# Performance work log

Hardware: AMD Instinct MI355X
Metric: run time of the kernel (lower is better)

The kernel has to match this reference:

```python
import jax, jax.numpy as jnp
import numpy as np

CH = 512
GROUPS = 32
EPS = 1e-5
B, H, W = 4, 64, 64


def setup_inputs() -> dict:
    key = jax.random.key(0)
    ks = jax.random.split(key, 6)
    s = 1.0 / np.sqrt(CH)  # conv2d default init scale (approx, uniform fan-in)
    return {
        "x": jax.random.normal(ks[0], (B, CH, H, W), dtype=jnp.float32),
        "norm_w": jnp.ones((CH,), jnp.float32),
        "norm_b": jnp.zeros((CH,), jnp.float32),
        "q_w": jax.random.normal(ks[1], (CH, CH), jnp.float32) * s,
        "q_b": jnp.zeros((CH,), jnp.float32),
        "k_w": jax.random.normal(ks[2], (CH, CH), jnp.float32) * s,
        "k_b": jnp.zeros((CH,), jnp.float32),
        "v_w": jax.random.normal(ks[3], (CH, CH), jnp.float32) * s,
        "v_b": jnp.zeros((CH,), jnp.float32),
        "proj_w": jax.random.normal(ks[4], (CH, CH), jnp.float32) * s,
        "proj_b": jnp.zeros((CH,), jnp.float32),
    }


def _group_norm(x, w, b):
    # x: [B, C, H, W]; 32 groups over channel dim
    bsz, c, h, wd = x.shape
    xg = x.reshape(bsz, GROUPS, c // GROUPS, h, wd)
    mean = xg.mean(axis=(2, 3, 4), keepdims=True)
    var = xg.var(axis=(2, 3, 4), keepdims=True)
    xg = (xg - mean) * jax.lax.rsqrt(var + EPS)
    x = xg.reshape(bsz, c, h, wd)
    return x * w[None, :, None, None] + b[None, :, None, None]


def _conv1x1(x, w, b):
    # x: [B, C, H, W], w: [O, C] -> [B, O, H, W]
    return jnp.einsum('bchw,oc->bohw', x, w) + b[None, :, None, None]


def reference(x, norm_w, norm_b, q_w, q_b, k_w, k_b, v_w, v_b, proj_w, proj_b):
    h = _group_norm(x, norm_w, norm_b)
    b, c, hh, ww = h.shape
    n = hh * ww
    q = _conv1x1(h, q_w, q_b).reshape(b, c, n).transpose(0, 2, 1)  # [b, n, c]
    k = _conv1x1(h, k_w, k_b).reshape(b, c, n)                     # [b, c, n]
    v = _conv1x1(h, v_w, v_b).reshape(b, c, n).transpose(0, 2, 1)  # [b, n, c]
    attn = jnp.einsum('bnc,bcm->bnm', q, k) * (c ** -0.5)          # [b, n, n]
    attn = jax.nn.softmax(attn, axis=-1)
    out = jnp.einsum('bnm,bmc->bnc', attn, v)                      # [b, n, c]
    out = out.transpose(0, 2, 1).reshape(b, c, hh, ww)
    return x + _conv1x1(out, proj_w, proj_b)
```

## Files before the change

### kernel.cpp

```cpp
#include <hip/hip_runtime.h>

#define NB 4
#define CH 512
#define NPIX 4096
#define GSZ 16
#define KVB 32
#define NT (NPIX / KVB)
#define DYN_LDS 136192
#define GEMM_LDS 65536

typedef __attribute__((ext_vector_type(8))) short bf16x8;
typedef __attribute__((ext_vector_type(4))) short bf16x4;
typedef __attribute__((ext_vector_type(4))) float f32x4;

#define MFMA __builtin_amdgcn_mfma_f32_16x16x32_bf16

static __device__ __forceinline__ short f2bf(float f) {
  unsigned u = __builtin_bit_cast(unsigned, f);
  u += 0x7fffu + ((u >> 16) & 1u);
  return (short)(u >> 16);
}

static __device__ __forceinline__ float bperm_f(int srclane, float v) {
  int r = __builtin_amdgcn_ds_bpermute(srclane << 2, __builtin_bit_cast(int, v));
  return __builtin_bit_cast(float, r);
}

typedef __attribute__((address_space(1))) unsigned glob_u32;
typedef __attribute__((address_space(3))) unsigned lds_u32;
static __device__ __forceinline__ void gl_lds16(const void* g, void* l) {
  __builtin_amdgcn_global_load_lds((const glob_u32*)g, (lds_u32*)l, 16, 0, 0);
}

__global__ __launch_bounds__(256) void wconv_kernel(
    const float* __restrict__ qw, const float* __restrict__ kw,
    const float* __restrict__ vw, const float* __restrict__ pw,
    short* __restrict__ wstack, short* __restrict__ wp) {
  int idx = (blockIdx.x * 256 + threadIdx.x) * 4;
  int mat = idx >> 18;
  int off = idx & 262143;
  const float* src = (mat == 0) ? qw : (mat == 1) ? kw : (mat == 2) ? vw : pw;
  short* dst = (mat < 3) ? (wstack + (size_t)mat * 262144) : wp;
  float4 v = *reinterpret_cast<const float4*>(src + off);
  bf16x4 o;
  o[0] = f2bf(v.x); o[1] = f2bf(v.y); o[2] = f2bf(v.z); o[3] = f2bf(v.w);
  *reinterpret_cast<bf16x4*>(dst + off) = o;
}

__global__ __launch_bounds__(256) void gn_kernel(
    const float* __restrict__ x, const float* __restrict__ nw,
    const float* __restrict__ nb, short* __restrict__ hT) {
  int pairid = blockIdx.x >> 1, half = blockIdx.x & 1;
  int b = pairid >> 5, g = pairid & 31;
  int tid = threadIdx.x;
  const float* base = x + (size_t)(b * CH + g * GSZ) * NPIX;
  const float4* b4 = reinterpret_cast<const float4*>(base);
  float s = 0.f, s2 = 0.f;
  for (int i = tid; i < GSZ * NPIX / 4; i += 256) {
    float4 v = b4[i];
    s += v.x + v.y + v.z + v.w;
    s2 += v.x * v.x + v.y * v.y + v.z * v.z + v.w * v.w;
  }
  #pragma unroll
  for (int m = 1; m < 64; m <<= 1) { s += __shfl_xor(s, m); s2 += __shfl_xor(s2, m); }
  __shared__ float red[8];
  if ((tid & 63) == 0) { red[(tid >> 6) * 2] = s; red[(tid >> 6) * 2 + 1] = s2; }
  __syncthreads();
  s = red[0] + red[2] + red[4] + red[6];
  s2 = red[1] + red[3] + red[5] + red[7];
  float mean = s * (1.f / 65536.f);
  float var = s2 * (1.f / 65536.f) - mean * mean;
  float rstd = rsqrtf(var + 1e-5f);
  int c = tid >> 4, nq = tid & 15;
  float wch = nw[g * GSZ + c] * rstd;
  float bch = nb[g * GSZ + c] - mean * wch;
  __shared__ short lt[GSZ][264];
  short* outb = hT + (size_t)b * NPIX * CH + g * GSZ;
  const float* srcc = base + (size_t)c * NPIX + nq * 16;
  for (int chunk = half * 8; chunk < half * 8 + 8; ++chunk) {
    const float4* sp = reinterpret_cast<const float4*>(srcc + chunk * 256);
    float4 v0 = sp[0], v1 = sp[1], v2 = sp[2], v3 = sp[3];
    bf16x8 w0, w1;
    w0[0] = f2bf(v0.x * wch + bch); w0[1] = f2bf(v0.y * wch + bch);
    w0[2] = f2bf(v0.z * wch + bch); w0[3] = f2bf(v0.w * wch + bch);
    w0[4] = f2bf(v1.x * wch + bch); w0[5] = f2bf(v1.y * wch + bch);
    w0[6] = f2bf(v1.z * wch + bch); w0[7] = f2bf(v1.w * wch + bch);
    w1[0] = f2bf(v2.x * wch + bch); w1[1] = f2bf(v2.y * wch + bch);
    w1[2] = f2bf(v2.z * wch + bch); w1[3] = f2bf(v2.w * wch + bch);
    w1[4] = f2bf(v3.x * wch + bch); w1[5] = f2bf(v3.y * wch + bch);
    w1[6] = f2bf(v3.z * wch + bch); w1[7] = f2bf(v3.w * wch + bch);
    *reinterpret_cast<bf16x8*>(&lt[c][nq * 16]) = w0;
    *reinterpret_cast<bf16x8*>(&lt[c][nq * 16 + 8]) = w1;
    __syncthreads();
    bf16x8 o0, o1;
    #pragma unroll
    for (int cc = 0; cc < 8; ++cc) o0[cc] = lt[cc][tid];
    #pragma unroll
    for (int cc = 0; cc < 8; ++cc) o1[cc] = lt[cc + 8][tid];
    short* orow = outb + (size_t)(chunk * 256 + tid) * CH;
    *reinterpret_cast<bf16x8*>(orow) = o0;
    *reinterpret_cast<bf16x8*>(orow + 8) = o1;
    __syncthreads();
  }
}

__global__ __launch_bounds__(256) void qkv_kernel(
    const short* __restrict__ wstack, const short* __restrict__ hT,
    const float* __restrict__ qb, const float* __restrict__ kb,
    const float* __restrict__ vb,
    short* __restrict__ qT, short* __restrict__ kT, short* __restrict__ vC) {
  extern __shared__ char qsm[];
  char* abuf = qsm;
  char* bbuf = qsm + 32768;

  int b = blockIdx.z;
  int by = blockIdx.x;
  int nbase = blockIdx.y * 128;
  int tid = threadIdx.x;
  int lane = tid & 63, wid = tid >> 6;
  int l15 = lane & 15, lg = lane >> 4;
  int wr = wid >> 1, wc = wid & 1;

  const short* arows = wstack + (size_t)by * 128 * CH;
  const short* brows = hT + ((size_t)b * NPIX + nbase) * CH;

  auto stage = [&](int buf, int kidx) {
    char* ad = abuf + buf * 16384;
    char* bd = bbuf + buf * 16384;
    #pragma unroll
    for (int i = 0; i < 4; ++i) {
      int off = i * 4096 + tid * 16;
      int row = off >> 7;
      int c16 = (off >> 4) & 7;
      int gchunk = (c16 ^ (row & 7)) * 8;
      gl_lds16(arows + (size_t)row * CH + kidx * 64 + gchunk, ad + off);
      gl_lds16(brows + (size_t)row * CH + kidx * 64 + gchunk, bd + off);
    }
  };

  f32x4 acc[4][4];
  #pragma unroll
  for (int mi = 0; mi < 4; ++mi)
    #pragma unroll
    for (int ni = 0; ni < 4; ++ni) acc[mi][ni] = (f32x4){0.f, 0.f, 0.f, 0.f};

  stage(0, 0);
  __syncthreads();

  int cur = 0;
  for (int kt = 0; kt < 8; ++kt) {
    if (kt + 1 < 8) stage(cur ^ 1, kt + 1);
    const char* ab = abuf + cur * 16384;
    const char* bb = bbuf + cur * 16384;
    #pragma unroll
    for (int ks = 0; ks < 2; ++ks) {
      bf16x8 af[4], bf[4];
      #pragma unroll
      for (int mi = 0; mi < 4; ++mi) {
        int row = wr * 64 + mi * 16 + l15;
        af[mi] = *reinterpret_cast<const bf16x8*>(
            ab + row * 128 + (((ks * 4 + lg) ^ (row & 7)) << 4));
      }
      #pragma unroll
      for (int ni = 0; ni < 4; ++ni) {
        int row = wc * 64 + ni * 16 + l15;
        bf[ni] = *reinterpret_cast<const bf16x8*>(
            bb + row * 128 + (((ks * 4 + lg) ^ (row & 7)) << 4));
      }
      #pragma unroll
      for (int mi = 0; mi < 4; ++mi)
        #pragma unroll
        for (int ni = 0; ni < 4; ++ni)
          acc[mi][ni] = MFMA(af[mi], bf[ni], acc[mi][ni], 0, 0, 0);
    }
    __syncthreads();
    cur ^= 1;
  }

  int oglob = by * 128;
  #pragma unroll
  for (int mi = 0; mi < 4; ++mi) {
    int oo = oglob + wr * 64 + mi * 16 + lg * 4;
    #pragma unroll
    for (int ni = 0; ni < 4; ++ni) {
      int nn = nbase + wc * 64 + ni * 16 + l15;
      f32x4 a = acc[mi][ni];
      if (oglob < 1024) {
        const float* bias = (oglob < 512) ? qb : kb;
        short* dstm = (oglob < 512) ? qT : kT;
        float sc = (oglob < 512) ? 0.044194173824159216f : 1.0f;
        int ol = oo & 511;
        bf16x4 pk;
        #pragma unroll
        for (int r = 0; r < 4; ++r) pk[r] = f2bf((a[r] + bias[ol + r]) * sc);
        *reinterpret_cast<bf16x4*>(dstm + ((size_t)b * NPIX + nn) * CH + ol) = pk;
      } else {
        int ov = oo - 1024;
        short* dstv = vC + ((size_t)b * CH + ov) * NPIX + nn;
        #pragma unroll
        for (int r = 0; r < 4; ++r) dstv[(size_t)r * NPIX] = f2bf(a[r] + vb[ov + r]);
      }
    }
  }
}

__global__ __launch_bounds__(512, 2) void flash_kernel(
    const short* __restrict__ qT, const short* __restrict__ kT,
    const short* __restrict__ vC, short* __restrict__ ao) {
  extern __shared__ char smem[];
  char* kbuf = smem;
  char* vbuf = smem + 65536;
  char* pbuf = smem + 131072;
  float* exch = (float*)(smem + 135168);

  int lin = blockIdx.y * 64 + blockIdx.x;
  int sw = (lin & 7) * 32 + (lin >> 3);
  int qb = sw & 63, b = sw >> 6;

  int tid = threadIdx.x;
  int lane = tid & 63, w = tid >> 6;
  int p = w >> 1, h = w & 1;
  int l15 = lane & 15, lg = lane >> 4;
  int qrow = qb * 64 + p * 16;

  const short* qptr = qT + ((size_t)b * NPIX + qrow + l15) * CH + lg * 8;
  bf16x8 qf[16];
  #pragma unroll
  for (int ks = 0; ks < 16; ++ks) qf[ks] = *reinterpret_cast<const bf16x8*>(qptr + ks * 32);

  f32x4 oacc[16];
  #pragma unroll
  for (int i = 0; i < 16; ++i) oacc[i] = (f32x4){0.f, 0.f, 0.f, 0.f};
  float mrow = -INFINITY, lrow = 0.f;
  bf16x8 pa_prev;
  bf16x8 vf_prev[16];
  #pragma unroll
  for (int i = 0; i < 8; ++i) pa_prev[i] = 0;
  #pragma unroll
  for (int j = 0; j < 16; ++j)
    #pragma unroll
    for (int i = 0; i < 8; ++i) vf_prev[j][i] = 0;

  const short* kTb = kT + (size_t)b * NPIX * CH;
  const short* vCb = vC + (size_t)b * CH * NPIX;
  const int swz = (l15 & 7) << 4;
  const int vswz = ((l15 >> 1) & 3) << 4;
  const int pswz = (l15 & 3) << 4;
  char* ppair = pbuf + p * 1024;
  float* exw = exch + (w * 16 + l15) * 2;
  float* exr = exch + ((w ^ 1) * 16 + l15) * 2;

  auto stage = [&](int buf, int t) {
    int m0 = t * KVB;
    char* kd = kbuf + buf * 32768;
    char* vd = vbuf + buf * 32768;
    #pragma unroll
    for (int i = 0; i < 4; ++i) {
      int r = w * 4 + i;
      const short* src = kTb + (size_t)(m0 + r) * CH + ((lane ^ (r & 7)) * 8);
      gl_lds16(src, kd + r * 1024);
    }
    #pragma unroll
    for (int i = 0; i < 4; ++i) {
      int j = w * 4 + i;
      int ch = j * 16 + (lane >> 2);
      const short* src = vCb + (size_t)ch * NPIX + m0 +
                         (((lane & 3) ^ ((lane >> 3) & 3)) * 8);
      gl_lds16(src, vd + j * 1024);
    }
  };

  stage(0, 0);
  asm volatile("s_waitcnt vmcnt(0)" ::: "memory");
  __syncthreads();

  int cur = 0;
  for (int t = 0; t < NT; ++t) {
    const char* kb_ = kbuf + cur * 32768;
    const char* vb_ = vbuf + cur * 32768;
    if (t + 1 < NT) stage(cur ^ 1, t + 1);
    f32x4 sa = (f32x4){0.f, 0.f, 0.f, 0.f};
    f32x4 sb = (f32x4){0.f, 0.f, 0.f, 0.f};
    __builtin_amdgcn_s_setprio(1);
    #pragma unroll
    for (int cs = 0; cs < 16; cs += 2) {
      bf16x8 kf0 = *reinterpret_cast<const bf16x8*>(
          kb_ + (h * 16 + l15) * 1024 + ((cs * 64 + lg * 16) ^ swz));
      bf16x8 kf1 = *reinterpret_cast<const bf16x8*>(
          kb_ + (h * 16 + l15) * 1024 + (((cs + 1) * 64 + lg * 16) ^ swz));
      sa = MFMA(kf0, qf[cs], sa, 0, 0, 0);
      sb = MFMA(kf1, qf[cs + 1], sb, 0, 0, 0);
    }
    __builtin_amdgcn_s_setprio(0);
    f32x4 st = sa + sb;
    float tmax = fmaxf(fmaxf(st[0], st[1]), fmaxf(st[2], st[3]));
    tmax = fmaxf(tmax, __shfl_xor(tmax, 16));
    tmax = fmaxf(tmax, __shfl_xor(tmax, 32));
    float pr[4];
    float psh;
    pr[0] = __expf(st[0] - tmax); pr[1] = __expf(st[1] - tmax);
    pr[2] = __expf(st[2] - tmax); pr[3] = __expf(st[3] - tmax);
    psh = (pr[0] + pr[1]) + (pr[2] + pr[3]);
    psh += __shfl_xor(psh, 16);
    psh += __shfl_xor(psh, 32);
    if (lane < 16) { exw[0] = tmax; exw[1] = psh; }
    asm volatile("s_waitcnt lgkmcnt(0)" ::: "memory");
    __builtin_amdgcn_s_barrier();
    __builtin_amdgcn_sched_barrier(0);
    float mo = exr[0], po = exr[1];
    float mnew = fmaxf(mrow, fmaxf(tmax, mo));
    float alpha = __expf(mrow - mnew);
    float scl = __expf(tmax - mnew);
    lrow = lrow * alpha + psh * scl + po * __expf(mo - mnew);
    mrow = mnew;
    {
      bf16x4 pk;
      pk[0] = f2bf(pr[0] * scl); pk[1] = f2bf(pr[1] * scl);
      pk[2] = f2bf(pr[2] * scl); pk[3] = f2bf(pr[3] * scl);
      *reinterpret_cast<bf16x4*>(ppair + l15 * 64 + ((h * 32 + lg * 8) ^ pswz)) = pk;
    }
    __builtin_amdgcn_s_setprio(1);
    #pragma unroll
    for (int j = 0; j < 16; ++j)
      oacc[j] = MFMA(pa_prev, vf_prev[j], oacc[j], 0, 0, 0);
    __builtin_amdgcn_s_setprio(0);
    if (!__all(alpha == 1.0f)) {
      float a4[4];
      #pragma unroll
      for (int r = 0; r < 4; ++r) a4[r] = bperm_f(lg * 4 + r, alpha);
      #pragma unroll
      for (int j = 0; j < 16; ++j) {
        oacc[j][0] *= a4[0]; oacc[j][1] *= a4[1];
        oacc[j][2] *= a4[2]; oacc[j][3] *= a4[3];
      }
    }
    #pragma unroll
    for (int j = 0; j < 16; ++j)
      vf_prev[j] = *reinterpret_cast<const bf16x8*>(
          vb_ + ((h * 16 + j) * 16 + l15) * 64 + ((lg * 16) ^ vswz));
    asm volatile("s_waitcnt vmcnt(0) lgkmcnt(0)" ::: "memory");
    __builtin_amdgcn_s_barrier();
    __builtin_amdgcn_sched_barrier(0);
    pa_prev = *reinterpret_cast<const bf16x8*>(ppair + l15 * 64 + ((lg * 16) ^ pswz));
    cur ^= 1;
  }
  #pragma unroll
  for (int j = 0; j < 16; ++j)
    oacc[j] = MFMA(pa_prev, vf_prev[j], oacc[j], 0, 0, 0);

  float linv = 1.f / lrow;
  float r4[4];
  #pragma unroll
  for (int r = 0; r < 4; ++r) r4[r] = bperm_f(lg * 4 + r, linv);
  short* aob = ao + ((size_t)b * NPIX + qrow) * CH;
  #pragma unroll
  for (int j = 0; j < 16; ++j) {
    int cb2 = h * 16 + j;
    #pragma unroll
    for (int r = 0; r < 4; ++r) {
      aob[(size_t)(lg * 4 + r) * CH + cb2 * 16 + l15] = f2bf(oacc[j][r] * r4[r]);
    }
  }
}

__global__ __launch_bounds__(256) void proj_kernel(
    const short* __restrict__ wpm, const short* __restrict__ ao,
    const float* __restrict__ x, const float* __restrict__ pb,
    float* __restrict__ out) {
  extern __shared__ char qsm[];
  char* abuf = qsm;
  char* bbuf = qsm + 32768;

  int b = blockIdx.z;
  int by = blockIdx.x;
  int nbase = blockIdx.y * 128;
  int tid = threadIdx.x;
  int lane = tid & 63, wid = tid >> 6;
  int l15 = lane & 15, lg = lane >> 4;
  int wr = wid >> 1, wc = wid & 1;

  const short* arows = wpm + (size_t)by * 128 * CH;
  const short* brows = ao + ((size_t)b * NPIX + nbase) * CH;

  auto stage = [&](int buf, int kidx) {
    char* ad = abuf + buf * 16384;
    char* bd = bbuf + buf * 16384;
    #pragma unroll
    for (int i = 0; i < 4; ++i) {
      int off = i * 4096 + tid * 16;
      int row = off >> 7;
      int c16 = (off >> 4) & 7;
      int gchunk = (c16 ^ (row & 7)) * 8;
      gl_lds16(arows + (size_t)row * CH + kidx * 64 + gchunk, ad + off);
      gl_lds16(brows + (size_t)row * CH + kidx * 64 + gchunk, bd + off);
    }
  };

  f32x4 acc[4][4];
  #pragma unroll
  for (int mi = 0; mi < 4; ++mi)
    #pragma unroll
    for (int ni = 0; ni < 4; ++ni) acc[mi][ni] = (f32x4){0.f, 0.f, 0.f, 0.f};

  stage(0, 0);
  __syncthreads();

  int cur = 0;
  for (int kt = 0; kt < 8; ++kt) {
    if (kt + 1 < 8) stage(cur ^ 1, kt + 1);
    const char* ab = abuf + cur * 16384;
    const char* bb = bbuf + cur * 16384;
    #pragma unroll
    for (int ks = 0; ks < 2; ++ks) {
      bf16x8 af[4], bf[4];
      #pragma unroll
      for (int mi = 0; mi < 4; ++mi) {
        int row = wr * 64 + mi * 16 + l15;
        af[mi] = *reinterpret_cast<const bf16x8*>(
            ab + row * 128 + (((ks * 4 + lg) ^ (row & 7)) << 4));
      }
      #pragma unroll
      for (int ni = 0; ni < 4; ++ni) {
        int row = wc * 64 + ni * 16 + l15;
        bf[ni] = *reinterpret_cast<const bf16x8*>(
            bb + row * 128 + (((ks * 4 + lg) ^ (row & 7)) << 4));
      }
      #pragma unroll
      for (int mi = 0; mi < 4; ++mi)
        #pragma unroll
        for (int ni = 0; ni < 4; ++ni)
          acc[mi][ni] = MFMA(af[mi], bf[ni], acc[mi][ni], 0, 0, 0);
    }
    __syncthreads();
    cur ^= 1;
  }

  #pragma unroll
  for (int mi = 0; mi < 4; ++mi) {
    int oo = by * 128 + wr * 64 + mi * 16 + lg * 4;
    #pragma unroll
    for (int ni = 0; ni < 4; ++ni) {
      int nn = nbase + wc * 64 + ni * 16 + l15;
      f32x4 a = acc[mi][ni];
      #pragma unroll
      for (int r = 0; r < 4; ++r) {
        size_t idx = ((size_t)b * CH + oo + r) * NPIX + nn;
        out[idx] = a[r] + pb[oo + r] + x[idx];
      }
    }
  }
}

extern "C" void kernel_launch(void* const* d_in, const int* in_sizes, int n_in,
                              void* d_out, int out_size, void* d_ws, size_t ws_size,
                              hipStream_t stream) {
  const float* x  = (const float*)d_in[0];
  const float* nw = (const float*)d_in[1];
  const float* nb = (const float*)d_in[2];
  const float* qw = (const float*)d_in[3];
  const float* qb = (const float*)d_in[4];
  const float* kw = (const float*)d_in[5];
  const float* kb = (const float*)d_in[6];
  const float* vw = (const float*)d_in[7];
  const float* vb = (const float*)d_in[8];
  const float* pw = (const float*)d_in[9];
  const float* pb = (const float*)d_in[10];
  char* ws = (char*)d_ws;
  short* wstack = (short*)(ws);
  short* wp     = (short*)(ws + 1572864);
  short* hT     = (short*)(ws + 2101248);
  short* qT     = (short*)(ws + 18878464);
  short* kT     = (short*)(ws + 35655680);
  short* vC     = (short*)(ws + 52432896);
  short* ao     = hT;
  float* out = (float*)d_out;

  hipFuncSetAttribute((const void*)flash_kernel,
                      hipFuncAttributeMaxDynamicSharedMemorySize, DYN_LDS);
  hipFuncSetAttribute((const void*)qkv_kernel,
                      hipFuncAttributeMaxDynamicSharedMemorySize, GEMM_LDS);
  hipFuncSetAttribute((const void*)proj_kernel,
                      hipFuncAttributeMaxDynamicSharedMemorySize, GEMM_LDS);

  wconv_kernel<<<1024, 256, 0, stream>>>(qw, kw, vw, pw, wstack, wp);
  gn_kernel<<<256, 256, 0, stream>>>(x, nw, nb, hT);
  qkv_kernel<<<dim3(12, 32, NB), 256, GEMM_LDS, stream>>>(wstack, hT, qb, kb, vb, qT, kT, vC);
  flash_kernel<<<dim3(64, NB), 512, DYN_LDS, stream>>>(qT, kT, vC, ao);
  proj_kernel<<<dim3(4, 32, NB), 256, GEMM_LDS, stream>>>(wp, ao, x, pb, out);
}
```

Before: 437.3 us.

## Split group norm into stats and apply kernels; XCD-aware GEMM block mapping

Group norm is split into a stats kernel that writes mean and rstd per (batch, group) to workspace, followed by an apply kernel with 512 blocks. The old kernel had every block recompute the full-group reduction. The qkv and proj GEMMs switch to a 1D grid remapped so that blocks sharing the same pixel tile land on the same XCD, to improve L2 reuse of the activation rows. The cost is one extra kernel launch and a second read of x.

```diff
diff --git a/kernel.cpp b/kernel.cpp
--- a/kernel.cpp
+++ b/kernel.cpp
@@ -47,14 +47,12 @@
   *reinterpret_cast<bf16x4*>(dst + off) = o;
 }
 
-__global__ __launch_bounds__(256) void gn_kernel(
-    const float* __restrict__ x, const float* __restrict__ nw,
-    const float* __restrict__ nb, short* __restrict__ hT) {
-  int pairid = blockIdx.x >> 1, half = blockIdx.x & 1;
-  int b = pairid >> 5, g = pairid & 31;
+__global__ __launch_bounds__(256) void gn_stats_kernel(
+    const float* __restrict__ x, float* __restrict__ st) {
+  int b = blockIdx.x >> 5, g = blockIdx.x & 31;
   int tid = threadIdx.x;
-  const float* base = x + (size_t)(b * CH + g * GSZ) * NPIX;
-  const float4* b4 = reinterpret_cast<const float4*>(base);
+  const float4* b4 = reinterpret_cast<const float4*>(
+      x + (size_t)(b * CH + g * GSZ) * NPIX);
   float s = 0.f, s2 = 0.f;
   for (int i = tid; i < GSZ * NPIX / 4; i += 256) {
     float4 v = b4[i];
@@ -66,18 +64,32 @@
   __shared__ float red[8];
   if ((tid & 63) == 0) { red[(tid >> 6) * 2] = s; red[(tid >> 6) * 2 + 1] = s2; }
   __syncthreads();
-  s = red[0] + red[2] + red[4] + red[6];
-  s2 = red[1] + red[3] + red[5] + red[7];
-  float mean = s * (1.f / 65536.f);
-  float var = s2 * (1.f / 65536.f) - mean * mean;
-  float rstd = rsqrtf(var + 1e-5f);
+  if (tid == 0) {
+    s = red[0] + red[2] + red[4] + red[6];
+    s2 = red[1] + red[3] + red[5] + red[7];
+    float mean = s * (1.f / 65536.f);
+    float var = s2 * (1.f / 65536.f) - mean * mean;
+    st[blockIdx.x * 2] = mean;
+    st[blockIdx.x * 2 + 1] = rsqrtf(var + 1e-5f);
+  }
+}
+
+__global__ __launch_bounds__(256) void gn_apply_kernel(
+    const float* __restrict__ x, const float* __restrict__ nw,
+    const float* __restrict__ nb, const float* __restrict__ st,
+    short* __restrict__ hT) {
+  int quarter = blockIdx.x & 3, pairid = blockIdx.x >> 2;
+  int b = pairid >> 5, g = pairid & 31;
+  int tid = threadIdx.x;
+  float mean = st[pairid * 2], rstd = st[pairid * 2 + 1];
   int c = tid >> 4, nq = tid & 15;
   float wch = nw[g * GSZ + c] * rstd;
   float bch = nb[g * GSZ + c] - mean * wch;
   __shared__ short lt[GSZ][264];
+  const float* base = x + (size_t)(b * CH + g * GSZ) * NPIX;
   short* outb = hT + (size_t)b * NPIX * CH + g * GSZ;
   const float* srcc = base + (size_t)c * NPIX + nq * 16;
-  for (int chunk = half * 8; chunk < half * 8 + 8; ++chunk) {
+  for (int chunk = quarter * 4; chunk < quarter * 4 + 4; ++chunk) {
     const float4* sp = reinterpret_cast<const float4*>(srcc + chunk * 256);
     float4 v0 = sp[0], v1 = sp[1], v2 = sp[2], v3 = sp[3];
     bf16x8 w0, w1;
@@ -113,9 +125,12 @@
   char* abuf = qsm;
   char* bbuf = qsm + 32768;
 
-  int b = blockIdx.z;
-  int by = blockIdx.x;
-  int nbase = blockIdx.y * 128;
+  int hwid = blockIdx.x;
+  int xcd = hwid & 7, slot = hwid >> 3;
+  int by = slot % 12, gq = slot / 12;
+  int grp = xcd + 8 * gq;
+  int b = grp >> 5;
+  int nbase = (grp & 31) * 128;
   int tid = threadIdx.x;
   int lane = tid & 63, wid = tid >> 6;
   int l15 = lane & 15, lg = lane >> 4;
@@ -371,9 +386,12 @@
   char* abuf = qsm;
   char* bbuf = qsm + 32768;
 
-  int b = blockIdx.z;
-  int by = blockIdx.x;
-  int nbase = blockIdx.y * 128;
+  int hwid = blockIdx.x;
+  int xcd = hwid & 7, slot = hwid >> 3;
+  int by = slot & 3, gq = slot >> 2;
+  int grp = xcd + 8 * gq;
+  int b = grp >> 5;
+  int nbase = (grp & 31) * 128;
   int tid = threadIdx.x;
   int lane = tid & 63, wid = tid >> 6;
   int l15 = lane & 15, lg = lane >> 4;
@@ -468,6 +486,7 @@
   char* ws = (char*)d_ws;
   short* wstack = (short*)(ws);
   short* wp     = (short*)(ws + 1572864);
+  float* gnstat = (float*)(ws + 2097152);
   short* hT     = (short*)(ws + 2101248);
   short* qT     = (short*)(ws + 18878464);
   short* kT     = (short*)(ws + 35655680);
@@ -483,8 +502,9 @@
                       hipFuncAttributeMaxDynamicSharedMemorySize, GEMM_LDS);
 
   wconv_kernel<<<1024, 256, 0, stream>>>(qw, kw, vw, pw, wstack, wp);
-  gn_kernel<<<256, 256, 0, stream>>>(x, nw, nb, hT);
-  qkv_kernel<<<dim3(12, 32, NB), 256, GEMM_LDS, stream>>>(wstack, hT, qb, kb, vb, qT, kT, vC);
+  gn_stats_kernel<<<128, 256, 0, stream>>>(x, gnstat);
+  gn_apply_kernel<<<512, 256, 0, stream>>>(x, nw, nb, gnstat, hT);
+  qkv_kernel<<<1536, 256, GEMM_LDS, stream>>>(wstack, hT, qb, kb, vb, qT, kT, vC);
   flash_kernel<<<dim3(64, NB), 512, DYN_LDS, stream>>>(qT, kT, vC, ao);
-  proj_kernel<<<dim3(4, 32, NB), 256, GEMM_LDS, stream>>>(wp, ao, x, pb, out);
-}
+  proj_kernel<<<512, 256, GEMM_LDS, stream>>>(wp, ao, x, pb, out);
+}
```

Result: no change. 435.2 us (-0.5%).
